# Optimization experiments

Measured on AMD Instinct MI355X. Metric: run time of the kernel, lower is better.

Reference implementation:

```python
import jax, jax.numpy as jnp
import numpy as np

N = 50000
E = 800000
F_IN, F_HID, F_OUT = 128, 64, 64
NUM_AS = 12  # 4 aggregators * 3 scalers
EPS = 1e-5


def _glorot(key, shape):
    return jax.random.normal(key, shape, jnp.float32) * (1.0 / np.sqrt(shape[0]))


def setup_inputs() -> dict:
    key = jax.random.key(0)
    ks = jax.random.split(key, 16)
    inp = {}
    inp['x'] = jax.random.normal(ks[0], (N, F_IN), jnp.float32)
    inp['edge_index'] = jax.random.randint(ks[1], (2, E), 0, N, dtype=jnp.int32)
    dims = [(F_IN, F_HID), (F_HID, F_HID), (F_HID, F_OUT)]
    k = 2
    for i, (fi, fo) in enumerate(dims):
        inp[f'pre_w{i}'] = _glorot(ks[k], (2 * fi, fi)); k += 1
        inp[f'pre_b{i}'] = jnp.zeros((fi,), jnp.float32)
        inp[f'post_w{i}'] = _glorot(ks[k], ((NUM_AS + 1) * fi, fo)); k += 1
        inp[f'post_b{i}'] = jnp.zeros((fo,), jnp.float32)
        inp[f'lin_w{i}'] = _glorot(ks[k], (fo, fo)); k += 1
        inp[f'lin_b{i}'] = jnp.zeros((fo,), jnp.float32)
    inp['skip_w0'] = _glorot(ks[k], (F_IN, F_HID))
    inp['skip_b0'] = jnp.zeros((F_HID,), jnp.float32)
    return inp


def _forward(x, edge_index, params):
    src, dst = edge_index[0], edge_index[1]
    # in-degree per destination node (PNA scalers use the target-node degree)
    counts = jax.ops.segment_sum(jnp.ones((E,), jnp.float32), dst, N)
    avg_log = jnp.mean(jnp.log1p(counts))  # avg_deg['log'] from degree histogram
    deg = jnp.maximum(counts, 1.0)         # clamp(1) as in DegreeScalerAggregation
    logdeg = jnp.log(deg + 1.0)
    amp = (logdeg / avg_log)[:, None]
    att = (avg_log / logdeg)[:, None]
    has = (counts > 0.0)[:, None]

    def conv(h_in, pw, pb, ow, ob, lw, lb):
        # message: pre_nn(concat([x_i, x_j])) per edge  -> [E, F]
        h = jnp.concatenate([h_in[dst], h_in[src]], axis=-1) @ pw + pb
        s1 = jax.ops.segment_sum(h, dst, N)
        s2 = jax.ops.segment_sum(h * h, dst, N)
        mean = s1 / deg[:, None]
        var = s2 / deg[:, None] - mean * mean
        std = jnp.sqrt(jax.nn.relu(var) + EPS)
        mn = jnp.where(has, jax.ops.segment_min(h, dst, N), 0.0)
        mx = jnp.where(has, jax.ops.segment_max(h, dst, N), 0.0)
        agg = jnp.concatenate([mean, mn, mx, std], axis=-1)          # [N, 4F]
        scaled = jnp.concatenate([agg, agg * amp, agg * att], axis=-1)  # [N, 12F]
        u = jnp.concatenate([h_in, scaled], axis=-1) @ ow + ob       # post_nn
        return u @ lw + lb                                           # final lin

    (pw0, pb0, ow0, ob0, lw0, lb0,
     pw1, pb1, ow1, ob1, lw1, lb1,
     pw2, pb2, ow2, ob2, lw2, lb2, sw0, sb0) = params
    # layer 0: skip is Linear(128 -> 64); dropout is identity in eval mode
    h = jax.nn.elu(conv(x, pw0, pb0, ow0, ob0, lw0, lb0) + (x @ sw0 + sb0))
    # layers 1, 2: skip is Identity (matching channels)
    h = jax.nn.elu(conv(h, pw1, pb1, ow1, ob1, lw1, lb1) + h)
    h = jax.nn.elu(conv(h, pw2, pb2, ow2, ob2, lw2, lb2) + h)
    return h


def reference(x, edge_index,
              pre_w0, pre_b0, post_w0, post_b0, lin_w0, lin_b0,
              pre_w1, pre_b1, post_w1, post_b1, lin_w1, lin_b1,
              pre_w2, pre_b2, post_w2, post_b2, lin_w2, lin_b2,
              skip_w0, skip_b0):
    params = (pre_w0, pre_b0, post_w0, post_b0, lin_w0, lin_b0,
              pre_w1, pre_b1, post_w1, post_b1, lin_w1, lin_b1,
              pre_w2, pre_b2, post_w2, post_b2, lin_w2, lin_b2,
              skip_w0, skip_b0)
    return _forward(x, edge_index, params)
```

## Files before the change

### kernel.cpp

```cpp
#include <hip/hip_runtime.h>
#include <math.h>

#define NN 50000
#define NE 800000

__global__ void zero_counts_kernel(int* counts) {
  int i = blockIdx.x * blockDim.x + threadIdx.x;
  if (i < NN) counts[i] = 0;
}

__global__ void count_kernel(const int* __restrict__ dst, int* __restrict__ counts) {
  int e = blockIdx.x * blockDim.x + threadIdx.x;
  if (e < NE) atomicAdd(&counts[dst[e]], 1);
}

__global__ void scan_kernel(const int* __restrict__ counts, int* __restrict__ rowptr,
                            int* __restrict__ cursor, float* __restrict__ scal) {
  __shared__ int sdata[1024];
  __shared__ int s_carry;
  __shared__ float wsum[16];
  int t = threadIdx.x;
  if (t == 0) s_carry = 0;
  __syncthreads();
  float logsum = 0.f;
  for (int base = 0; base < NN; base += 1024) {
    int i = base + t;
    int c = (i < NN) ? counts[i] : 0;
    if (i < NN) logsum += log1pf((float)c);
    sdata[t] = c;
    __syncthreads();
    for (int off = 1; off < 1024; off <<= 1) {
      int v = (t >= off) ? sdata[t - off] : 0;
      __syncthreads();
      sdata[t] += v;
      __syncthreads();
    }
    int incl = sdata[t];
    int tot = sdata[1023];
    int excl = incl - c;
    if (i < NN) { int r = s_carry + excl; rowptr[i] = r; cursor[i] = r; }
    __syncthreads();
    if (t == 0) s_carry += tot;
    __syncthreads();
  }
  if (t == 0) rowptr[NN] = s_carry;
  for (int off = 32; off > 0; off >>= 1) logsum += __shfl_down(logsum, off, 64);
  if ((t & 63) == 0) wsum[t >> 6] = logsum;
  __syncthreads();
  if (t == 0) {
    float s = 0.f;
    for (int i = 0; i < 16; i++) s += wsum[i];
    scal[0] = s / (float)NN;
  }
}

__global__ void degs_kernel(const int* __restrict__ counts, const float* __restrict__ scal,
                            float* __restrict__ amp, float* __restrict__ att) {
  int i = blockIdx.x * blockDim.x + threadIdx.x;
  if (i < NN) {
    float deg = fmaxf((float)counts[i], 1.f);
    float ld = logf(deg + 1.f);
    float al = scal[0];
    amp[i] = ld / al;
    att[i] = al / ld;
  }
}

__global__ void scatter_kernel(const int* __restrict__ src, const int* __restrict__ dst,
                               int* __restrict__ cursor, int* __restrict__ ssrc) {
  int e = blockIdx.x * blockDim.x + threadIdx.x;
  if (e < NE) {
    int p = atomicAdd(&cursor[dst[e]], 1);
    ssrc[p] = src[e];
  }
}

__global__ __launch_bounds__(256, 4) void gemm64_kernel(
    const float* __restrict__ A, int lda, int K,
    const float* __restrict__ W, int ldw,
    const float* __restrict__ bias,
    float* __restrict__ C, int ldc) {
  __shared__ __align__(16) float As[64][36];
  __shared__ __align__(16) float Ws[32][68];
  int t = threadIdx.x;
  int n0 = blockIdx.x * 64;
  int nq = (t >> 4) * 4, cq = (t & 15) * 4;
  float acc[4][4] = {};
  for (int k0 = 0; k0 < K; k0 += 32) {
#pragma unroll
    for (int i = 0; i < 2; i++) {
      int fl = t + i * 256;
      int nl = fl >> 3, f4 = fl & 7;
      int row = n0 + nl; if (row >= NN) row = NN - 1;
      *(float4*)&As[nl][f4 * 4] = *(const float4*)&A[(size_t)row * lda + k0 + f4 * 4];
    }
#pragma unroll
    for (int i = 0; i < 2; i++) {
      int fl = t + i * 256;
      int kl = fl >> 4, c4 = fl & 15;
      *(float4*)&Ws[kl][c4 * 4] = *(const float4*)&W[(size_t)(k0 + kl) * ldw + c4 * 4];
    }
    __syncthreads();
#pragma unroll
    for (int k = 0; k < 32; k++) {
      float4 w = *(const float4*)&Ws[k][cq];
      float wv[4] = {w.x, w.y, w.z, w.w};
      float av[4] = {As[nq + 0][k], As[nq + 1][k], As[nq + 2][k], As[nq + 3][k]};
#pragma unroll
      for (int i = 0; i < 4; i++)
#pragma unroll
        for (int j = 0; j < 4; j++) acc[i][j] += av[i] * wv[j];
    }
    __syncthreads();
  }
#pragma unroll
  for (int i = 0; i < 4; i++) {
    int n = n0 + nq + i;
    if (n < NN) {
      float4 o = make_float4(acc[i][0], acc[i][1], acc[i][2], acc[i][3]);
      if (bias) {
        float4 b4 = *(const float4*)&bias[cq];
        o.x += b4.x; o.y += b4.y; o.z += b4.z; o.w += b4.w;
      }
      *(float4*)&C[(size_t)n * ldc + cq] = o;
    }
  }
}

template <int F>
__global__ __launch_bounds__(256) void agg_kernel(
    const float* __restrict__ pd, const float* __restrict__ ps,
    const int* __restrict__ rowptr, const int* __restrict__ ssrc,
    float* __restrict__ agg) {
  constexpr int C = F / 64;
  int lane = threadIdx.x & 63;
  int wid = threadIdx.x >> 6;
  int n = blockIdx.x * 4 + wid;
  if (n >= NN) return;
  int beg = rowptr[n], end = rowptr[n + 1];
  float pdv[C], sum[C], sq[C], mn[C], mx[C];
#pragma unroll
  for (int c = 0; c < C; c++) {
    pdv[c] = pd[(size_t)n * F + lane + 64 * c];
    sum[c] = 0.f; sq[c] = 0.f; mn[c] = INFINITY; mx[c] = -INFINITY;
  }
  for (int e = beg; e < end; e++) {
    int s = ssrc[e];
#pragma unroll
    for (int c = 0; c < C; c++) {
      float h = pdv[c] + ps[(size_t)s * F + lane + 64 * c];
      sum[c] += h; sq[c] += h * h;
      mn[c] = fminf(mn[c], h); mx[c] = fmaxf(mx[c], h);
    }
  }
  int cnt = end - beg;
  float deg = fmaxf((float)cnt, 1.f);
  float inv = 1.f / deg;
#pragma unroll
  for (int c = 0; c < C; c++) {
    float mean = sum[c] * inv;
    float var = sq[c] * inv - mean * mean;
    float sd = sqrtf(fmaxf(var, 0.f) + 1e-5f);
    float mnv = cnt > 0 ? mn[c] : 0.f;
    float mxv = cnt > 0 ? mx[c] : 0.f;
    size_t b = (size_t)n * 4 * F + lane + 64 * c;
    agg[b] = mean;
    agg[b + F] = mnv;
    agg[b + 2 * F] = mxv;
    agg[b + 3 * F] = sd;
  }
}

template <int F>
__global__ __launch_bounds__(256, 4) void post_kernel(
    const float* __restrict__ h_in, const float* __restrict__ agg,
    const float* __restrict__ amp, const float* __restrict__ att,
    const float* __restrict__ pw, const float* __restrict__ pb,
    const float* __restrict__ lw, const float* __restrict__ lb,
    const float* __restrict__ skip, float* __restrict__ out) {
  __shared__ __align__(16) char lds_pool[(64 * 36 + 32 * 68) * 4];
  float (*Xs)[36] = (float(*)[36])lds_pool;
  float (*Ws)[68] = (float(*)[68])(lds_pool + 64 * 36 * 4);
  float (*Us)[68] = (float(*)[68])lds_pool;
  __shared__ __align__(16) float Lws[64][68];
  __shared__ float s_amp[64], s_att[64];

  int t = threadIdx.x;
  int n0 = blockIdx.x * 64;

  const float4* lw4 = (const float4*)lw;
#pragma unroll
  for (int i = 0; i < 4; i++) {
    int fl = t + i * 256;
    *(float4*)&Lws[fl >> 4][(fl & 15) * 4] = lw4[fl];
  }
  if (t < 64) {
    int n = n0 + t; if (n >= NN) n = NN - 1;
    s_amp[t] = amp[n];
    s_att[t] = att[n];
  }
  __syncthreads();

  int nq = (t >> 4) * 4, cq = (t & 15) * 4;
  float acc[4][4] = {};
  const int KT = 13 * F;
  for (int k0 = 0; k0 < KT; k0 += 32) {
    const float* src; int ldx, koff, mode;
    if (k0 < F)          { src = h_in; ldx = F;     koff = k0;         mode = 0; }
    else if (k0 < 5 * F) { src = agg;  ldx = 4 * F; koff = k0 - F;     mode = 0; }
    else if (k0 < 9 * F) { src = agg;  ldx = 4 * F; koff = k0 - 5 * F; mode = 1; }
    else                 { src = agg;  ldx = 4 * F; koff = k0 - 9 * F; mode = 2; }
#pragma unroll
    for (int i = 0; i < 2; i++) {
      int fl = t + i * 256;
      int nl = fl >> 3, f4 = fl & 7;
      int n = n0 + nl; if (n >= NN) n = NN - 1;
      float4 v = *(const float4*)&src[(size_t)n * ldx + koff + f4 * 4];
      float s = (mode == 0) ? 1.f : (mode == 1 ? s_amp[nl] : s_att[nl]);
      v.x *= s; v.y *= s; v.z *= s; v.w *= s;
      *(float4*)&Xs[nl][f4 * 4] = v;
    }
    const float4* wp4 = (const float4*)(pw + (size_t)k0 * 64);
#pragma unroll
    for (int i = 0; i < 2; i++) {
      int fl = t + i * 256;
      *(float4*)&Ws[fl >> 4][(fl & 15) * 4] = wp4[fl];
    }
    __syncthreads();
#pragma unroll
    for (int k = 0; k < 32; k++) {
      float4 w = *(const float4*)&Ws[k][cq];
      float wv[4] = {w.x, w.y, w.z, w.w};
      float av[4] = {Xs[nq + 0][k], Xs[nq + 1][k], Xs[nq + 2][k], Xs[nq + 3][k]};
#pragma unroll
      for (int i = 0; i < 4; i++)
#pragma unroll
        for (int j = 0; j < 4; j++) acc[i][j] += av[i] * wv[j];
    }
    __syncthreads();
  }

  float4 pb4 = *(const float4*)&pb[cq];
#pragma unroll
  for (int i = 0; i < 4; i++) {
    float4 u = make_float4(acc[i][0] + pb4.x, acc[i][1] + pb4.y,
                           acc[i][2] + pb4.z, acc[i][3] + pb4.w);
    *(float4*)&Us[nq + i][cq] = u;
  }
  __syncthreads();

  float acc2[4][4] = {};
#pragma unroll
  for (int k = 0; k < 64; k++) {
    float4 w = *(const float4*)&Lws[k][cq];
    float wv[4] = {w.x, w.y, w.z, w.w};
    float av[4] = {Us[nq + 0][k], Us[nq + 1][k], Us[nq + 2][k], Us[nq + 3][k]};
#pragma unroll
    for (int i = 0; i < 4; i++)
#pragma unroll
      for (int j = 0; j < 4; j++) acc2[i][j] += av[i] * wv[j];
  }

  float4 lb4 = *(const float4*)&lb[cq];
#pragma unroll
  for (int i = 0; i < 4; i++) {
    int n = n0 + nq + i;
    if (n < NN) {
      float4 sk4 = *(const float4*)&skip[(size_t)n * 64 + cq];
      float v0 = acc2[i][0] + lb4.x + sk4.x;
      float v1 = acc2[i][1] + lb4.y + sk4.y;
      float v2 = acc2[i][2] + lb4.z + sk4.z;
      float v3 = acc2[i][3] + lb4.w + sk4.w;
      float4 o = make_float4(v0 > 0.f ? v0 : expm1f(v0),
                             v1 > 0.f ? v1 : expm1f(v1),
                             v2 > 0.f ? v2 : expm1f(v2),
                             v3 > 0.f ? v3 : expm1f(v3));
      *(float4*)&out[(size_t)n * 64 + cq] = o;
    }
  }
}

extern "C" void kernel_launch(void* const* d_in, const int* in_sizes, int n_in,
                              void* d_out, int out_size, void* d_ws, size_t ws_size,
                              hipStream_t stream) {
  const float* x = (const float*)d_in[0];
  const int* ei = (const int*)d_in[1];
  const int* esrc = ei;
  const int* edst = ei + NE;
  const float* pre_w[3]  = {(const float*)d_in[2],  (const float*)d_in[8],  (const float*)d_in[14]};
  const float* pre_b[3]  = {(const float*)d_in[3],  (const float*)d_in[9],  (const float*)d_in[15]};
  const float* post_w[3] = {(const float*)d_in[4],  (const float*)d_in[10], (const float*)d_in[16]};
  const float* post_b[3] = {(const float*)d_in[5],  (const float*)d_in[11], (const float*)d_in[17]};
  const float* lin_w[3]  = {(const float*)d_in[6],  (const float*)d_in[12], (const float*)d_in[18]};
  const float* lin_b[3]  = {(const float*)d_in[7],  (const float*)d_in[13], (const float*)d_in[19]};
  const float* skip_w = (const float*)d_in[20];
  const float* skip_b = (const float*)d_in[21];

  char* p = (char*)d_ws;
  auto alloc = [&](size_t b) { char* r = p; p += (b + 255) & ~(size_t)255; return r; };
  int* counts  = (int*)alloc((size_t)NN * 4);
  int* rowptr  = (int*)alloc((size_t)(NN + 1) * 4);
  int* cursor  = (int*)alloc((size_t)NN * 4);
  int* ssrc    = (int*)alloc((size_t)NE * 4);
  float* amp   = (float*)alloc((size_t)NN * 4);
  float* att   = (float*)alloc((size_t)NN * 4);
  float* scal  = (float*)alloc(256);
  float* pd    = (float*)alloc((size_t)NN * 128 * 4);
  float* ps    = (float*)alloc((size_t)NN * 128 * 4);
  float* agg   = (float*)alloc((size_t)NN * 512 * 4);
  float* ha    = (float*)alloc((size_t)NN * 64 * 4);
  float* hb    = (float*)alloc((size_t)NN * 64 * 4);
  float* sk    = (float*)alloc((size_t)NN * 64 * 4);
  (void)ws_size; (void)in_sizes; (void)n_in; (void)out_size;

  zero_counts_kernel<<<(NN + 255) / 256, 256, 0, stream>>>(counts);
  count_kernel<<<(NE + 255) / 256, 256, 0, stream>>>(edst, counts);
  scan_kernel<<<1, 1024, 0, stream>>>(counts, rowptr, cursor, scal);
  degs_kernel<<<(NN + 255) / 256, 256, 0, stream>>>(counts, scal, amp, att);
  scatter_kernel<<<(NE + 255) / 256, 256, 0, stream>>>(esrc, edst, cursor, ssrc);

  int gn = (NN + 63) / 64;

  gemm64_kernel<<<gn, 256, 0, stream>>>(x, 128, 128, skip_w, 64, skip_b, sk, 64);

  gemm64_kernel<<<gn, 256, 0, stream>>>(x, 128, 128, pre_w[0],           128, pre_b[0],      pd,      128);
  gemm64_kernel<<<gn, 256, 0, stream>>>(x, 128, 128, pre_w[0] + 64,      128, pre_b[0] + 64, pd + 64, 128);
  gemm64_kernel<<<gn, 256, 0, stream>>>(x, 128, 128, pre_w[0] + 128*128,      128, nullptr,  ps,      128);
  gemm64_kernel<<<gn, 256, 0, stream>>>(x, 128, 128, pre_w[0] + 128*128 + 64, 128, nullptr,  ps + 64, 128);
  agg_kernel<128><<<(NN + 3) / 4, 256, 0, stream>>>(pd, ps, rowptr, ssrc, agg);
  post_kernel<128><<<gn, 256, 0, stream>>>(x, agg, amp, att, post_w[0], post_b[0],
                                           lin_w[0], lin_b[0], sk, ha);

  gemm64_kernel<<<gn, 256, 0, stream>>>(ha, 64, 64, pre_w[1],         64, pre_b[1], pd, 64);
  gemm64_kernel<<<gn, 256, 0, stream>>>(ha, 64, 64, pre_w[1] + 64*64, 64, nullptr,  ps, 64);
  agg_kernel<64><<<(NN + 3) / 4, 256, 0, stream>>>(pd, ps, rowptr, ssrc, agg);
  post_kernel<64><<<gn, 256, 0, stream>>>(ha, agg, amp, att, post_w[1], post_b[1],
                                          lin_w[1], lin_b[1], ha, hb);

  gemm64_kernel<<<gn, 256, 0, stream>>>(hb, 64, 64, pre_w[2],         64, pre_b[2], pd, 64);
  gemm64_kernel<<<gn, 256, 0, stream>>>(hb, 64, 64, pre_w[2] + 64*64, 64, nullptr,  ps, 64);
  agg_kernel<64><<<(NN + 3) / 4, 256, 0, stream>>>(pd, ps, rowptr, ssrc, agg);
  post_kernel<64><<<gn, 256, 0, stream>>>(hb, agg, amp, att, post_w[2], post_b[2],
                                          lin_w[2], lin_b[2], hb, (float*)d_out);
}
```

Baseline: 2.894 ms.

## Fuse paired pre-GEMMs and reuse agg tile across three scaler weight slices

Adds a dual-output GEMM kernel that computes two 64-column weight slices from a single load of the A tile, halving reads of the node features and the kernel launches for the pre-message projections. The post kernel is restructured so each aggregate tile is loaded once and multiplied by the identity, amplification and attenuation weight blocks together. The amp/att scaling is applied to the accumulators afterwards, which cuts agg reads from three passes to one. The cost is more accumulator registers and more LDS per block, which can lower occupancy.

Result: faster. 2.819 ms (-2.6%).

```diff
diff --git a/kernel.cpp b/kernel.cpp
--- a/kernel.cpp
+++ b/kernel.cpp
@@ -127,6 +127,78 @@
   }
 }
 
+__global__ __launch_bounds__(256, 4) void gemm_dual_kernel(
+    const float* __restrict__ A, int lda, int K,
+    const float* __restrict__ W1, const float* __restrict__ W2, int ldw,
+    const float* __restrict__ b1, const float* __restrict__ b2,
+    float* __restrict__ C1, int ldc1, float* __restrict__ C2, int ldc2) {
+  __shared__ __align__(16) float As[64][36];
+  __shared__ __align__(16) float Ws[32][132];
+  int t = threadIdx.x;
+  int n0 = blockIdx.x * 64;
+  int nq = (t >> 4) * 4;
+  int cq = (t & 15) * 8;
+  float acc[4][8] = {};
+  for (int k0 = 0; k0 < K; k0 += 32) {
+#pragma unroll
+    for (int i = 0; i < 2; i++) {
+      int fl = t + i * 256;
+      int nl = fl >> 3, f4 = fl & 7;
+      int row = n0 + nl; if (row >= NN) row = NN - 1;
+      *(float4*)&As[nl][f4 * 4] = *(const float4*)&A[(size_t)row * lda + k0 + f4 * 4];
+    }
+#pragma unroll
+    for (int i = 0; i < 2; i++) {
+      int fl = t + i * 256;
+      int kl = fl >> 4, c4 = (fl & 15) * 4;
+      *(float4*)&Ws[kl][c4] = *(const float4*)&W1[(size_t)(k0 + kl) * ldw + c4];
+    }
+#pragma unroll
+    for (int i = 0; i < 2; i++) {
+      int fl = t + i * 256;
+      int kl = fl >> 4, c4 = (fl & 15) * 4;
+      *(float4*)&Ws[kl][64 + c4] = *(const float4*)&W2[(size_t)(k0 + kl) * ldw + c4];
+    }
+    __syncthreads();
+#pragma unroll
+    for (int k = 0; k < 32; k++) {
+      float av[4] = {As[nq + 0][k], As[nq + 1][k], As[nq + 2][k], As[nq + 3][k]};
+      float4 wl = *(const float4*)&Ws[k][cq];
+      float4 wh = *(const float4*)&Ws[k][cq + 4];
+      float wv[8] = {wl.x, wl.y, wl.z, wl.w, wh.x, wh.y, wh.z, wh.w};
+#pragma unroll
+      for (int i = 0; i < 4; i++)
+#pragma unroll
+        for (int j = 0; j < 8; j++) acc[i][j] += av[i] * wv[j];
+    }
+    __syncthreads();
+  }
+  bool hi = (t & 15) >= 8;
+  float* Cd = hi ? C2 : C1;
+  int ldc = hi ? ldc2 : ldc1;
+  const float* bs = hi ? b2 : b1;
+  int col = hi ? cq - 64 : cq;
+  float bv[8] = {};
+  if (bs) {
+    float4 blo = *(const float4*)&bs[col];
+    float4 bhi = *(const float4*)&bs[col + 4];
+    bv[0] = blo.x; bv[1] = blo.y; bv[2] = blo.z; bv[3] = blo.w;
+    bv[4] = bhi.x; bv[5] = bhi.y; bv[6] = bhi.z; bv[7] = bhi.w;
+  }
+#pragma unroll
+  for (int i = 0; i < 4; i++) {
+    int n = n0 + nq + i;
+    if (n < NN) {
+      float4 lo = make_float4(acc[i][0] + bv[0], acc[i][1] + bv[1],
+                              acc[i][2] + bv[2], acc[i][3] + bv[3]);
+      float4 hi4 = make_float4(acc[i][4] + bv[4], acc[i][5] + bv[5],
+                               acc[i][6] + bv[6], acc[i][7] + bv[7]);
+      *(float4*)&Cd[(size_t)n * ldc + col] = lo;
+      *(float4*)&Cd[(size_t)n * ldc + col + 4] = hi4;
+    }
+  }
+}
+
 template <int F>
 __global__ __launch_bounds__(256) void agg_kernel(
     const float* __restrict__ pd, const float* __restrict__ ps,
@@ -178,64 +250,91 @@
     const float* __restrict__ pw, const float* __restrict__ pb,
     const float* __restrict__ lw, const float* __restrict__ lb,
     const float* __restrict__ skip, float* __restrict__ out) {
-  __shared__ __align__(16) char lds_pool[(64 * 36 + 32 * 68) * 4];
-  float (*Xs)[36] = (float(*)[36])lds_pool;
-  float (*Ws)[68] = (float(*)[68])(lds_pool + 64 * 36 * 4);
-  float (*Us)[68] = (float(*)[68])lds_pool;
-  __shared__ __align__(16) float Lws[64][68];
+  __shared__ __align__(16) float pool[64 * 36 + 3 * 32 * 68];
+  float (*Xs)[36] = (float(*)[36])pool;
+  float (*WAs)[68] = (float(*)[68])(pool + 64 * 36);
+  float (*WBs)[68] = (float(*)[68])(pool + 64 * 36 + 32 * 68);
+  float (*WCs)[68] = (float(*)[68])(pool + 64 * 36 + 2 * 32 * 68);
+  float (*Us)[68] = (float(*)[68])pool;
+  float (*Lws)[68] = (float(*)[68])(pool + 64 * 36 + 32 * 68);
   __shared__ float s_amp[64], s_att[64];
 
   int t = threadIdx.x;
   int n0 = blockIdx.x * 64;
-
-  const float4* lw4 = (const float4*)lw;
-#pragma unroll
-  for (int i = 0; i < 4; i++) {
-    int fl = t + i * 256;
-    *(float4*)&Lws[fl >> 4][(fl & 15) * 4] = lw4[fl];
-  }
   if (t < 64) {
     int n = n0 + t; if (n >= NN) n = NN - 1;
     s_amp[t] = amp[n];
     s_att[t] = att[n];
   }
-  __syncthreads();
 
   int nq = (t >> 4) * 4, cq = (t & 15) * 4;
-  float acc[4][4] = {};
-  const int KT = 13 * F;
-  for (int k0 = 0; k0 < KT; k0 += 32) {
-    const float* src; int ldx, koff, mode;
-    if (k0 < F)          { src = h_in; ldx = F;     koff = k0;         mode = 0; }
-    else if (k0 < 5 * F) { src = agg;  ldx = 4 * F; koff = k0 - F;     mode = 0; }
-    else if (k0 < 9 * F) { src = agg;  ldx = 4 * F; koff = k0 - 5 * F; mode = 1; }
-    else                 { src = agg;  ldx = 4 * F; koff = k0 - 9 * F; mode = 2; }
+  float accA[4][4] = {}, accB[4][4] = {}, accC[4][4] = {};
+
+  for (int k0 = 0; k0 < F; k0 += 32) {
 #pragma unroll
     for (int i = 0; i < 2; i++) {
       int fl = t + i * 256;
       int nl = fl >> 3, f4 = fl & 7;
       int n = n0 + nl; if (n >= NN) n = NN - 1;
-      float4 v = *(const float4*)&src[(size_t)n * ldx + koff + f4 * 4];
-      float s = (mode == 0) ? 1.f : (mode == 1 ? s_amp[nl] : s_att[nl]);
-      v.x *= s; v.y *= s; v.z *= s; v.w *= s;
-      *(float4*)&Xs[nl][f4 * 4] = v;
-    }
-    const float4* wp4 = (const float4*)(pw + (size_t)k0 * 64);
-#pragma unroll
-    for (int i = 0; i < 2; i++) {
-      int fl = t + i * 256;
-      *(float4*)&Ws[fl >> 4][(fl & 15) * 4] = wp4[fl];
+      *(float4*)&Xs[nl][f4 * 4] = *(const float4*)&h_in[(size_t)n * F + k0 + f4 * 4];
+    }
+    const float4* wa4 = (const float4*)(pw + (size_t)k0 * 64);
+#pragma unroll
+    for (int i = 0; i < 2; i++) {
+      int fl = t + i * 256;
+      *(float4*)&WAs[fl >> 4][(fl & 15) * 4] = wa4[fl];
     }
     __syncthreads();
 #pragma unroll
     for (int k = 0; k < 32; k++) {
-      float4 w = *(const float4*)&Ws[k][cq];
+      float4 w = *(const float4*)&WAs[k][cq];
       float wv[4] = {w.x, w.y, w.z, w.w};
       float av[4] = {Xs[nq + 0][k], Xs[nq + 1][k], Xs[nq + 2][k], Xs[nq + 3][k]};
 #pragma unroll
       for (int i = 0; i < 4; i++)
 #pragma unroll
-        for (int j = 0; j < 4; j++) acc[i][j] += av[i] * wv[j];
+        for (int j = 0; j < 4; j++) accA[i][j] += av[i] * wv[j];
+    }
+    __syncthreads();
+  }
+
+  for (int k0 = 0; k0 < 4 * F; k0 += 32) {
+#pragma unroll
+    for (int i = 0; i < 2; i++) {
+      int fl = t + i * 256;
+      int nl = fl >> 3, f4 = fl & 7;
+      int n = n0 + nl; if (n >= NN) n = NN - 1;
+      *(float4*)&Xs[nl][f4 * 4] = *(const float4*)&agg[(size_t)n * 4 * F + k0 + f4 * 4];
+    }
+    const float4* wa4 = (const float4*)(pw + (size_t)(F + k0) * 64);
+    const float4* wb4 = (const float4*)(pw + (size_t)(5 * F + k0) * 64);
+    const float4* wc4 = (const float4*)(pw + (size_t)(9 * F + k0) * 64);
+#pragma unroll
+    for (int i = 0; i < 2; i++) {
+      int fl = t + i * 256;
+      int kl = fl >> 4, c16 = (fl & 15) * 4;
+      *(float4*)&WAs[kl][c16] = wa4[fl];
+      *(float4*)&WBs[kl][c16] = wb4[fl];
+      *(float4*)&WCs[kl][c16] = wc4[fl];
+    }
+    __syncthreads();
+#pragma unroll
+    for (int k = 0; k < 32; k++) {
+      float av[4] = {Xs[nq + 0][k], Xs[nq + 1][k], Xs[nq + 2][k], Xs[nq + 3][k]};
+      float4 wa = *(const float4*)&WAs[k][cq];
+      float4 wb = *(const float4*)&WBs[k][cq];
+      float4 wc = *(const float4*)&WCs[k][cq];
+      float wav[4] = {wa.x, wa.y, wa.z, wa.w};
+      float wbv[4] = {wb.x, wb.y, wb.z, wb.w};
+      float wcv[4] = {wc.x, wc.y, wc.z, wc.w};
+#pragma unroll
+      for (int i = 0; i < 4; i++)
+#pragma unroll
+        for (int j = 0; j < 4; j++) {
+          accA[i][j] += av[i] * wav[j];
+          accB[i][j] += av[i] * wbv[j];
+          accC[i][j] += av[i] * wcv[j];
+        }
     }
     __syncthreads();
   }
@@ -243,9 +342,18 @@
   float4 pb4 = *(const float4*)&pb[cq];
 #pragma unroll
   for (int i = 0; i < 4; i++) {
-    float4 u = make_float4(acc[i][0] + pb4.x, acc[i][1] + pb4.y,
-                           acc[i][2] + pb4.z, acc[i][3] + pb4.w);
+    float a_ = s_amp[nq + i], t_ = s_att[nq + i];
+    float4 u = make_float4(accA[i][0] + a_ * accB[i][0] + t_ * accC[i][0] + pb4.x,
+                           accA[i][1] + a_ * accB[i][1] + t_ * accC[i][1] + pb4.y,
+                           accA[i][2] + a_ * accB[i][2] + t_ * accC[i][2] + pb4.z,
+                           accA[i][3] + a_ * accB[i][3] + t_ * accC[i][3] + pb4.w);
     *(float4*)&Us[nq + i][cq] = u;
+  }
+  const float4* lw4 = (const float4*)lw;
+#pragma unroll
+  for (int i = 0; i < 4; i++) {
+    int fl = t + i * 256;
+    *(float4*)&Lws[fl >> 4][(fl & 15) * 4] = lw4[fl];
   }
   __syncthreads();
 
@@ -323,22 +431,23 @@
 
   gemm64_kernel<<<gn, 256, 0, stream>>>(x, 128, 128, skip_w, 64, skip_b, sk, 64);
 
-  gemm64_kernel<<<gn, 256, 0, stream>>>(x, 128, 128, pre_w[0],           128, pre_b[0],      pd,      128);
-  gemm64_kernel<<<gn, 256, 0, stream>>>(x, 128, 128, pre_w[0] + 64,      128, pre_b[0] + 64, pd + 64, 128);
-  gemm64_kernel<<<gn, 256, 0, stream>>>(x, 128, 128, pre_w[0] + 128*128,      128, nullptr,  ps,      128);
-  gemm64_kernel<<<gn, 256, 0, stream>>>(x, 128, 128, pre_w[0] + 128*128 + 64, 128, nullptr,  ps + 64, 128);
+  gemm_dual_kernel<<<gn, 256, 0, stream>>>(x, 128, 128,
+      pre_w[0], pre_w[0] + 64, 128, pre_b[0], pre_b[0] + 64, pd, 128, pd + 64, 128);
+  gemm_dual_kernel<<<gn, 256, 0, stream>>>(x, 128, 128,
+      pre_w[0] + 128 * 128, pre_w[0] + 128 * 128 + 64, 128, nullptr, nullptr,
+      ps, 128, ps + 64, 128);
   agg_kernel<128><<<(NN + 3) / 4, 256, 0, stream>>>(pd, ps, rowptr, ssrc, agg);
   post_kernel<128><<<gn, 256, 0, stream>>>(x, agg, amp, att, post_w[0], post_b[0],
                                            lin_w[0], lin_b[0], sk, ha);
 
-  gemm64_kernel<<<gn, 256, 0, stream>>>(ha, 64, 64, pre_w[1],         64, pre_b[1], pd, 64);
-  gemm64_kernel<<<gn, 256, 0, stream>>>(ha, 64, 64, pre_w[1] + 64*64, 64, nullptr,  ps, 64);
+  gemm_dual_kernel<<<gn, 256, 0, stream>>>(ha, 64, 64,
+      pre_w[1], pre_w[1] + 64 * 64, 64, pre_b[1], nullptr, pd, 64, ps, 64);
   agg_kernel<64><<<(NN + 3) / 4, 256, 0, stream>>>(pd, ps, rowptr, ssrc, agg);
   post_kernel<64><<<gn, 256, 0, stream>>>(ha, agg, amp, att, post_w[1], post_b[1],
                                           lin_w[1], lin_b[1], ha, hb);
 
-  gemm64_kernel<<<gn, 256, 0, stream>>>(hb, 64, 64, pre_w[2],         64, pre_b[2], pd, 64);
-  gemm64_kernel<<<gn, 256, 0, stream>>>(hb, 64, 64, pre_w[2] + 64*64, 64, nullptr,  ps, 64);
+  gemm_dual_kernel<<<gn, 256, 0, stream>>>(hb, 64, 64,
+      pre_w[2], pre_w[2] + 64 * 64, 64, pre_b[2], nullptr, pd, 64, ps, 64);
   agg_kernel<64><<<(NN + 3) / 4, 256, 0, stream>>>(pd, ps, rowptr, ssrc, agg);
   post_kernel<64><<<gn, 256, 0, stream>>>(hb, agg, amp, att, post_w[2], post_b[2],
                                           lin_w[2], lin_b[2], hb, (float*)d_out);
```
